# Performance work log

Measured on AMD Instinct MI355X. Metric: run time of the kernel, lower is better.

Reference implementation:

```python
import jax, jax.numpy as jnp
import numpy as np

H = 1024
A = H // 2
B = 32
S = 1024
T = 1024


def setup_inputs() -> dict:
    key = jax.random.key(0)
    ks = jax.random.split(key, 16)
    sc = 0.02
    inp = {
        "hidden": jax.random.normal(ks[0], (1, B, H), jnp.float32),
        "encoder_hiddens": jax.random.normal(ks[1], (S, B, H), jnp.float32),
        "h0_s": jax.random.normal(ks[2], (T, B, H), jnp.float32),
        "ax": jax.random.uniform(ks[3], (B, S, 1), jnp.float32),
        # weights: torch Linear(in,out,bias=False) -> W has shape [out,in], y = x @ W.T
        "W1": jax.random.normal(ks[4], (A, H), jnp.float32) * sc,
        "W2": jax.random.normal(ks[5], (A, H), jnp.float32) * sc,
        "W3": jax.random.normal(ks[6], (A, 1), jnp.float32) * sc,
        "W4": jax.random.normal(ks[7], (1, 3 * A), jnp.float32) * sc,
        "W5": jax.random.normal(ks[8], (A, H), jnp.float32) * sc,
        "W6": jax.random.normal(ks[9], (A, H), jnp.float32) * sc,
        "W7": jax.random.normal(ks[10], (A, H), jnp.float32) * sc,
        "W8": jax.random.normal(ks[11], (1, 3 * A), jnp.float32) * sc,
        "W9": jax.random.normal(ks[12], (H, H), jnp.float32) * sc,
        "W10": jax.random.normal(ks[13], (H, H), jnp.float32) * sc,
        "W11": jax.random.normal(ks[14], (1, 2 * H), jnp.float32) * sc,
    }
    return inp


def reference(hidden, encoder_hiddens, h0_s, ax,
              W1, W2, W3, W4, W5, W6, W7, W8, W9, W10, W11):
    h = hidden[0]  # [B,H], hidden.squeeze(0)

    # ---- encoder (x) attention with coverage, vectorized over S ----
    wx = jnp.einsum('sbh,ah->sba', encoder_hiddens, W1)          # [S,B,A]
    wxy = h @ W2.T                                               # [B,A]
    # Linear3 on ax[:, j] ([B,1]): outer product with W3 column
    wxr = ax[:, :, 0][:, :, None] * W3[:, 0][None, None, :]       # [B,S,A]
    wxr = jnp.transpose(wxr, (1, 0, 2))                           # [S,B,A]
    cat_x = jnp.tanh(jnp.concatenate(
        [wx, jnp.broadcast_to(wxy, (S,) + wxy.shape), wxr], axis=-1))  # [S,B,3A]
    exi = jnp.einsum('sbc,oc->bso', cat_x, W4)                    # [B,S,1]
    axi = jax.nn.softmax(exi, axis=1)                             # [B,S,1]
    cxi = jnp.einsum('bs,sbh->bh', axi[:, :, 0], encoder_hiddens)  # [B,H]
    ax_new = ax + axi

    # ---- decoder-history (t) attention, vectorized over T ----
    wt = jnp.einsum('tbh,ah->tba', h0_s, W5)                      # [T,B,A]
    wtx = cxi @ W6.T                                              # [B,A]
    wty = h @ W7.T                                                # [B,A]
    Tn = h0_s.shape[0]
    cat_t = jnp.tanh(jnp.concatenate(
        [wt,
         jnp.broadcast_to(wtx, (Tn,) + wtx.shape),
         jnp.broadcast_to(wty, (Tn,) + wty.shape)], axis=-1))     # [T,B,3A]
    eti = jnp.einsum('tbc,oc->bto', cat_t, W8)                    # [B,T,1]
    ati = jax.nn.softmax(eti, axis=1)
    cti = jnp.einsum('bt,tbh->bh', ati[:, :, 0], h0_s)            # [B,H]

    # ---- gated fusion ----
    gxi = jnp.tanh(cxi @ W9.T)
    gti = jnp.tanh(cti @ W10.T)
    zi = jax.nn.sigmoid(jnp.concatenate([cxi, cti], axis=1) @ W11.T)  # [B,1]
    ci = zi * gxi + (1.0 - zi) * gti                              # [B,H]
    return ci, ax_new
```

## Files before the change

kernel.cpp:

```cpp
#include <hip/hip_runtime.h>
#include <hip/hip_bf16.h>

#define HH 1024
#define AA 512
#define BB 32
#define SS 1024
#define TN 1024
#define M_ENC (SS*BB)
#define M_TOT ((SS+TN)*BB)
#define NCH 8

#define ABUF 8192

typedef __attribute__((ext_vector_type(8))) short short8;
typedef __attribute__((ext_vector_type(4))) float f4;

union bfu { __hip_bfloat16 h; unsigned short u; };
__device__ __forceinline__ unsigned int f2bu(float x) {
  bfu t; t.h = __float2bfloat16(x); return (unsigned int)t.u;
}
__device__ __forceinline__ unsigned short f2b(float x) {
  bfu t; t.h = __float2bfloat16(x); return t.u;
}
__device__ __forceinline__ float tanh_fast(float x) {
  float e = __expf(2.f * x);
  return 1.f - 2.f / (e + 1.f);
}

__global__ void prep_all(const float* __restrict__ W1, const float* __restrict__ W5,
                         const float* __restrict__ W3, const float* __restrict__ W4,
                         unsigned short* __restrict__ W1c, unsigned short* __restrict__ W5c,
                         float* __restrict__ C) {
  if (blockIdx.x < 512) {
    const float* __restrict__ W = (blockIdx.x < 256) ? W1 : W5;
    unsigned short* __restrict__ Wc = (blockIdx.x < 256) ? W1c : W5c;
    const int t = (blockIdx.x & 255) * 256 + threadIdx.x;
    const int lane = t & 63;
    const int rg = (t >> 6) & 31;
    const int kb = t >> 11;
    const int row = rg * 16 + (lane & 15);
    const int k = kb * 32 + ((lane >> 4) << 3);
    const float* src = W + (size_t)row * HH + k;
    f4 v0 = *(const f4*)(src);
    f4 v1 = *(const f4*)(src + 4);
    short8 o;
    o[0] = f2b(v0[0]); o[1] = f2b(v0[1]); o[2] = f2b(v0[2]); o[3] = f2b(v0[3]);
    o[4] = f2b(v1[0]); o[5] = f2b(v1[1]); o[6] = f2b(v1[2]); o[7] = f2b(v1[3]);
    *(short8*)(Wc + (size_t)t * 8) = o;
  } else {
    __shared__ float r1[256], r3[256], r5[256];
    const int tp = threadIdx.x;
    float s1 = 0.f, s3 = 0.f, s5 = 0.f;
    for (int a = tp; a < AA; a += 256) {
      const float w = W3[a], u = W4[2 * AA + a];
      const float w2 = w * w;
      s1 += u * w; s3 += u * w * w2; s5 += u * w * w2 * w2;
    }
    r1[tp] = s1; r3[tp] = s3; r5[tp] = s5;
    __syncthreads();
    for (int off = 128; off > 0; off >>= 1) {
      if (tp < off) { r1[tp] += r1[tp + off]; r3[tp] += r3[tp + off]; r5[tp] += r5[tp + off]; }
      __syncthreads();
    }
    if (tp == 0) { C[0] = r1[0]; C[1] = -r3[0] / 3.f; C[2] = r5[0] * (2.f / 15.f); }
  }
}

__global__ __launch_bounds__(512, 4)
void e1_gemm(const float* __restrict__ enc, const float* __restrict__ h0,
             const unsigned short* __restrict__ W1c, const unsigned short* __restrict__ W5c,
             const float* __restrict__ W4, const float* __restrict__ W8,
             float* __restrict__ e1s, float* __restrict__ e1t) {
  const int wg   = blockIdx.x;
  const int tid  = threadIdx.x;
  const int lane = tid & 63;
  const int colg = tid >> 6;
  const int l15  = lane & 15;
  const int lg   = lane >> 4;
  const int koff = (wg & 1) << 3;

  const bool is_enc = (wg * 64) < M_ENC;
  const float* __restrict__ Xg = is_enc ? enc : h0;
  const unsigned short* __restrict__ Wc = is_enc ? W1c : W5c;
  const float* __restrict__ Vg = is_enc ? W4 : W8;
  const int row0 = is_enc ? wg * 64 : wg * 64 - M_ENC;

  __shared__ char lds_raw[2 * ABUF];
  float* lred = (float*)lds_raw;

  f4 acc[4][4];
#pragma unroll
  for (int i = 0; i < 4; ++i)
#pragma unroll
    for (int j = 0; j < 4; ++j) acc[i][j] = (f4){0.f, 0.f, 0.f, 0.f};

  const int arow = tid >> 3;
  const int aq   = tid & 7;
  const float* ap = Xg + (size_t)(row0 + arow) * HH + aq * 4;
  const int slotS = (aq >> 1) ^ ((arow >> 1) & 3);
  const int aDst = arow * 64 + slotS * 16 + (aq & 1) * 8;

  const int aRd = l15 * 64 + ((lg ^ ((l15 >> 1) & 3)) << 4);

  const char* bp = (const char*)Wc + colg * 4096 + lane * 16;

  f4 an0, an1;
  short8 bfr[8];

#define ALOAD(k_) do {                                                        \
    an0 = *(const f4*)(ap + (k_) * 64);                                       \
    an1 = *(const f4*)(ap + (k_) * 64 + 32);                                  \
  } while (0)

#define AWR(bo_) do {                                                         \
    uint2 o0_, o1_;                                                           \
    o0_.x = f2bu(an0[0]) | (f2bu(an0[1]) << 16);                              \
    o0_.y = f2bu(an0[2]) | (f2bu(an0[3]) << 16);                              \
    o1_.x = f2bu(an1[0]) | (f2bu(an1[1]) << 16);                              \
    o1_.y = f2bu(an1[2]) | (f2bu(an1[3]) << 16);                              \
    *(uint2*)(lds_raw + (bo_) + aDst) = o0_;                                  \
    *(uint2*)(lds_raw + (bo_) + 4096 + aDst) = o1_;                           \
  } while (0)

#define BLOAD(kb2_) do {                                                      \
    const char* b_ = bp + (size_t)(kb2_) * 65536;                             \
    _Pragma("unroll")                                                         \
    for (int q_ = 0; q_ < 8; ++q_)                                            \
      bfr[q_] = *(const short8*)(b_ + (q_ >> 2) * 32768 + (q_ & 3) * 1024);   \
  } while (0)

#define COMPUTE(bo_) do {                                                     \
    const char* base_ = lds_raw + (bo_);                                      \
    _Pragma("unroll")                                                         \
    for (int ks_ = 0; ks_ < 2; ++ks_) {                                       \
      __builtin_amdgcn_s_setprio(1);                                          \
      _Pragma("unroll")                                                       \
      for (int rt = 0; rt < 4; ++rt) {                                        \
        short8 af_ = *(const short8*)(base_ + ks_ * 4096 + aRd + rt * 1024);  \
        _Pragma("unroll")                                                     \
        for (int cf = 0; cf < 4; ++cf)                                        \
          acc[rt][cf] = __builtin_amdgcn_mfma_f32_16x16x32_bf16(              \
              af_, bfr[ks_ * 4 + cf], acc[rt][cf], 0, 0, 0);                  \
      }                                                                       \
      __builtin_amdgcn_s_setprio(0);                                          \
    }                                                                         \
  } while (0)

#define SYNCA() do {                                                          \
    __builtin_amdgcn_sched_barrier(0);                                        \
    asm volatile("s_waitcnt lgkmcnt(0)" ::: "memory");                        \
    __builtin_amdgcn_s_barrier();                                             \
    __builtin_amdgcn_sched_barrier(0);                                        \
  } while (0)

  ALOAD(koff);
  AWR(0);
  ALOAD((1 + koff) & 15);
  SYNCA();

#pragma unroll 1
  for (int it = 0; it < 7; ++it) {
    const int kc0 = (2 * it + koff) & 15;
    const int ka2 = (2 * it + 2 + koff) & 15;
    const int kc1 = (2 * it + 1 + koff) & 15;
    const int ka3 = (2 * it + 3 + koff) & 15;
    AWR(ABUF); ALOAD(ka2); BLOAD(kc0); COMPUTE(0); SYNCA();
    AWR(0); ALOAD(ka3); BLOAD(kc1); COMPUTE(ABUF); SYNCA();
  }
  AWR(ABUF); BLOAD((14 + koff) & 15); COMPUTE(0); SYNCA();
  BLOAD((15 + koff) & 15); COMPUTE(ABUF);
#undef ALOAD
#undef AWR
#undef BLOAD
#undef COMPUTE
#undef SYNCA

  float vvv[4];
#pragma unroll
  for (int cf = 0; cf < 4; ++cf) vvv[cf] = Vg[colg * 64 + cf * 16 + l15];

  __syncthreads();
#pragma unroll
  for (int rt = 0; rt < 4; ++rt) {
    float ps[4] = {0.f, 0.f, 0.f, 0.f};
#pragma unroll
    for (int cf = 0; cf < 4; ++cf) {
      const float w = vvv[cf];
#pragma unroll
      for (int r = 0; r < 4; ++r) ps[r] += w * tanh_fast(acc[rt][cf][r]);
    }
#pragma unroll
    for (int r = 0; r < 4; ++r) {
#pragma unroll
      for (int off = 1; off < 16; off <<= 1) ps[r] += __shfl_xor(ps[r], off);
    }
    if (l15 == 0) {
#pragma unroll
      for (int r = 0; r < 4; ++r)
        lred[colg * 64 + rt * 16 + lg * 4 + r] = ps[r];
    }
  }
  __syncthreads();
  if (tid < 64) {
    float s = 0.f;
#pragma unroll
    for (int c = 0; c < 8; ++c) s += lred[c * 64 + tid];
    const int gr = row0 + tid;
    const int q = gr >> 5;
    const int b = gr & 31;
    if (is_enc) e1s[b * SS + q] = s;
    else        e1t[b * TN + q] = s;
  }
}

__global__ void softmax_both(const float* __restrict__ e1s, const float* __restrict__ e1t,
                             const float* __restrict__ ax, const float* __restrict__ C,
                             float* __restrict__ axi, float* __restrict__ ati,
                             float* __restrict__ axnew) {
  const int tid = threadIdx.x;
  __shared__ float red[256];
  if (blockIdx.x < BB) {
    const int b = blockIdx.x;
    const float c0 = C[0], c1 = C[1], c2 = C[2];
    float loc[4], xv[4];
    float m = -1e30f;
#pragma unroll
    for (int i = 0; i < 4; ++i) {
      const int s = i * 256 + tid;
      const float x = ax[b * SS + s];
      const float x2 = x * x;
      xv[i] = x;
      loc[i] = e1s[b * SS + s] + x * (c0 + x2 * (c1 + x2 * c2));
      m = fmaxf(m, loc[i]);
    }
    red[tid] = m; __syncthreads();
    for (int off = 128; off > 0; off >>= 1) {
      if (tid < off) red[tid] = fmaxf(red[tid], red[tid + off]);
      __syncthreads();
    }
    m = red[0]; __syncthreads();
    float sum = 0.f;
#pragma unroll
    for (int i = 0; i < 4; ++i) { loc[i] = __expf(loc[i] - m); sum += loc[i]; }
    red[tid] = sum; __syncthreads();
    for (int off = 128; off > 0; off >>= 1) {
      if (tid < off) red[tid] += red[tid + off];
      __syncthreads();
    }
    const float inv = 1.f / red[0];
#pragma unroll
    for (int i = 0; i < 4; ++i) {
      const int s = i * 256 + tid;
      const float a_ = loc[i] * inv;
      axi[b * SS + s] = a_;
      axnew[b * SS + s] = xv[i] + a_;
    }
  } else {
    const int b = blockIdx.x - BB;
    float loc[4];
    float m = -1e30f;
#pragma unroll
    for (int i = 0; i < 4; ++i) { loc[i] = e1t[b * TN + i * 256 + tid]; m = fmaxf(m, loc[i]); }
    red[tid] = m; __syncthreads();
    for (int off = 128; off > 0; off >>= 1) {
      if (tid < off) red[tid] = fmaxf(red[tid], red[tid + off]);
      __syncthreads();
    }
    m = red[0]; __syncthreads();
    float sum = 0.f;
#pragma unroll
    for (int i = 0; i < 4; ++i) { loc[i] = __expf(loc[i] - m); sum += loc[i]; }
    red[tid] = sum; __syncthreads();
    for (int off = 128; off > 0; off >>= 1) {
      if (tid < off) red[tid] += red[tid + off];
      __syncthreads();
    }
    const float inv = 1.f / red[0];
#pragma unroll
    for (int i = 0; i < 4; ++i) ati[b * TN + (i * 256 + tid)] = loc[i] * inv;
  }
}

__global__ void wpart2(const float* __restrict__ enc, const float* __restrict__ h0,
                       const float* __restrict__ axi, const float* __restrict__ ati,
                       float* __restrict__ partx, float* __restrict__ partt) {
  const int gb = blockIdx.x;
  const bool isx = gb < BB * NCH;
  const float* __restrict__ X = isx ? enc : h0;
  const float* __restrict__ w = isx ? axi : ati;
  float* __restrict__ part = isx ? partx : partt;
  const int idx = isx ? gb : gb - BB * NCH;
  const int b = idx / NCH, ch = idx % NCH;
  const int tid = threadIdx.x;
  __shared__ float ws[SS / NCH];
  if (tid < SS / NCH) ws[tid] = w[b * SS + ch * (SS / NCH) + tid];
  __syncthreads();
  f4 acc = (f4){0.f, 0.f, 0.f, 0.f};
  const float* base = X + ((size_t)(ch * (SS / NCH)) * BB + b) * HH + tid * 4;
#pragma unroll 4
  for (int i = 0; i < SS / NCH; ++i) {
    f4 x = *(const f4*)(base + (size_t)i * BB * HH);
    acc += ws[i] * x;
  }
  *(f4*)&part[((size_t)(b * NCH + ch)) * HH + tid * 4] = acc;
}

__global__ void wreduce2(const float* __restrict__ partx, const float* __restrict__ partt,
                         float* __restrict__ cxi, float* __restrict__ cti) {
  const int idx = blockIdx.x * 256 + threadIdx.x;
  const bool isx = idx < BB * HH;
  const float* __restrict__ part = isx ? partx : partt;
  float* __restrict__ outp = isx ? cxi : cti;
  const int j = isx ? idx : idx - BB * HH;
  const int b = j / HH, h = j % HH;
  float s = 0.f;
#pragma unroll
  for (int ch = 0; ch < NCH; ++ch) s += part[((size_t)(b * NCH + ch)) * HH + h];
  outp[j] = s;
}

__global__ void ci_kernel(const float* __restrict__ cxi, const float* __restrict__ cti,
                          const float* __restrict__ W9, const float* __restrict__ W10,
                          const float* __restrict__ W11, float* __restrict__ out_ci) {
  const int b = blockIdx.x >> 2, hb = blockIdx.x & 3, tid = threadIdx.x;
  const int h = hb * 256 + tid;
  __shared__ float cx[HH], ct[HH];
  __shared__ float zred[4];
  for (int i = tid; i < HH; i += 256) { cx[i] = cxi[b * HH + i]; ct[i] = cti[b * HH + i]; }
  __syncthreads();
  float zs = 0.f;
  for (int i = tid; i < HH; i += 256) zs += cx[i] * W11[i] + ct[i] * W11[HH + i];
  for (int off = 32; off > 0; off >>= 1) zs += __shfl_down(zs, off);
  if ((tid & 63) == 0) zred[tid >> 6] = zs;
  __syncthreads();
  const float zt = zred[0] + zred[1] + zred[2] + zred[3];
  const float z = 1.f / (1.f + __expf(-zt));

  const float* __restrict__ w9r  = W9  + (size_t)h * HH;
  const float* __restrict__ w10r = W10 + (size_t)h * HH;
  float gx = 0.f, gt = 0.f;
  for (int k = 0; k < HH; k += 4) {
    f4 a = *(const f4*)(w9r + k);
    f4 c = *(const f4*)(w10r + k);
    gx += cx[k] * a[0] + cx[k + 1] * a[1] + cx[k + 2] * a[2] + cx[k + 3] * a[3];
    gt += ct[k] * c[0] + ct[k + 1] * c[1] + ct[k + 2] * c[2] + ct[k + 3] * c[3];
  }
  out_ci[b * HH + h] = z * tanhf(gx) + (1.f - z) * tanhf(gt);
}

extern "C" void kernel_launch(void* const* d_in, const int* in_sizes, int n_in,
                              void* d_out, int out_size, void* d_ws, size_t ws_size,
                              hipStream_t stream) {
  const float* enc = (const float*)d_in[1];
  const float* h0  = (const float*)d_in[2];
  const float* ax  = (const float*)d_in[3];
  const float* W1  = (const float*)d_in[4];
  const float* W3  = (const float*)d_in[6];
  const float* W4  = (const float*)d_in[7];
  const float* W5  = (const float*)d_in[8];
  const float* W8  = (const float*)d_in[11];
  const float* W9  = (const float*)d_in[12];
  const float* W10 = (const float*)d_in[13];
  const float* W11 = (const float*)d_in[14];
  float* out = (float*)d_out;

  float* w = (float*)d_ws;
  unsigned short* W1c = (unsigned short*)w;
  unsigned short* W5c = (unsigned short*)(w + 262144);
  float* partx = w;
  float* partt = w + 262144;
  float* e1s   = w + 524288;
  float* e1t   = w + 557056;
  float* axi   = w + 589824;
  float* ati   = w + 622592;
  float* cxi   = w + 655360;
  float* cti   = w + 688128;
  float* Cpoly = w + 720896;

  prep_all<<<513, 256, 0, stream>>>(W1, W5, W3, W4, W1c, W5c, Cpoly);
  e1_gemm<<<M_TOT / 64, 512, 0, stream>>>(enc, h0, W1c, W5c, W4, W8, e1s, e1t);
  softmax_both<<<2 * BB, 256, 0, stream>>>(e1s, e1t, ax, Cpoly, axi, ati, out + BB * HH);
  wpart2<<<2 * BB * NCH, 256, 0, stream>>>(enc, h0, axi, ati, partx, partt);
  wreduce2<<<2 * BB * HH / 256, 256, 0, stream>>>(partx, partt, cxi, cti);
  ci_kernel<<<BB * 4, 256, 0, stream>>>(cxi, cti, W9, W10, W11, out);
}
```

Measured before the change: 209.5 us.

## Load A fragments directly from global into registers, dropping LDS staging

The GEMM in e1_gemm no longer stages the fp32 activation tile into a double-buffered LDS area with barriers. Each wave now reads its own A rows straight from global memory, converts them to bf16 in registers and feeds the MFMAs. The per-WG K-offset staggering is removed and launch bounds drop to 2 waves per SIMD to allow more registers. This removes LDS traffic and barriers, but all 8 waves in a workgroup now reload the same A rows from global/L2 (8x redundant reads), and occupancy is reduced.

```diff
diff --git a/kernel.cpp b/kernel.cpp
--- a/kernel.cpp
+++ b/kernel.cpp
@@ -9,8 +9,6 @@
 #define M_ENC (SS*BB)
 #define M_TOT ((SS+TN)*BB)
 #define NCH 8
-
-#define ABUF 8192
 
 typedef __attribute__((ext_vector_type(8))) short short8;
 typedef __attribute__((ext_vector_type(4))) float f4;
@@ -66,7 +64,7 @@
   }
 }
 
-__global__ __launch_bounds__(512, 4)
+__global__ __launch_bounds__(512, 2)
 void e1_gemm(const float* __restrict__ enc, const float* __restrict__ h0,
              const unsigned short* __restrict__ W1c, const unsigned short* __restrict__ W5c,
              const float* __restrict__ W4, const float* __restrict__ W8,
@@ -77,7 +75,6 @@
   const int colg = tid >> 6;
   const int l15  = lane & 15;
   const int lg   = lane >> 4;
-  const int koff = (wg & 1) << 3;
 
   const bool is_enc = (wg * 64) < M_ENC;
   const float* __restrict__ Xg = is_enc ? enc : h0;
@@ -85,8 +82,7 @@
   const float* __restrict__ Vg = is_enc ? W4 : W8;
   const int row0 = is_enc ? wg * 64 : wg * 64 - M_ENC;
 
-  __shared__ char lds_raw[2 * ABUF];
-  float* lred = (float*)lds_raw;
+  __shared__ float lred[512];
 
   f4 acc[4][4];
 #pragma unroll
@@ -94,92 +90,56 @@
 #pragma unroll
     for (int j = 0; j < 4; ++j) acc[i][j] = (f4){0.f, 0.f, 0.f, 0.f};
 
-  const int arow = tid >> 3;
-  const int aq   = tid & 7;
-  const float* ap = Xg + (size_t)(row0 + arow) * HH + aq * 4;
-  const int slotS = (aq >> 1) ^ ((arow >> 1) & 3);
-  const int aDst = arow * 64 + slotS * 16 + (aq & 1) * 8;
-
-  const int aRd = l15 * 64 + ((lg ^ ((l15 >> 1) & 3)) << 4);
+  const float* ap0 = Xg + (size_t)(row0 + l15) * HH + lg * 8;
+  const float* ap1 = ap0 + 16 * HH;
+  const float* ap2 = ap1 + 16 * HH;
+  const float* ap3 = ap2 + 16 * HH;
 
   const char* bp = (const char*)Wc + colg * 4096 + lane * 16;
 
-  f4 an0, an1;
-  short8 bfr[8];
-
-#define ALOAD(k_) do {                                                        \
-    an0 = *(const f4*)(ap + (k_) * 64);                                       \
-    an1 = *(const f4*)(ap + (k_) * 64 + 32);                                  \
+#define PACK8(d_, x0_, x1_) do {                                              \
+    unsigned int lo0_ = f2bu(x0_[0]) | (f2bu(x0_[1]) << 16);                  \
+    unsigned int hi0_ = f2bu(x0_[2]) | (f2bu(x0_[3]) << 16);                  \
+    unsigned int lo1_ = f2bu(x1_[0]) | (f2bu(x1_[1]) << 16);                  \
+    unsigned int hi1_ = f2bu(x1_[2]) | (f2bu(x1_[3]) << 16);                  \
+    d_[0] = (short)(lo0_ & 0xffff); d_[1] = (short)(lo0_ >> 16);              \
+    d_[2] = (short)(hi0_ & 0xffff); d_[3] = (short)(hi0_ >> 16);              \
+    d_[4] = (short)(lo1_ & 0xffff); d_[5] = (short)(lo1_ >> 16);              \
+    d_[6] = (short)(hi1_ & 0xffff); d_[7] = (short)(hi1_ >> 16);              \
   } while (0)
 
-#define AWR(bo_) do {                                                         \
-    uint2 o0_, o1_;                                                           \
-    o0_.x = f2bu(an0[0]) | (f2bu(an0[1]) << 16);                              \
-    o0_.y = f2bu(an0[2]) | (f2bu(an0[3]) << 16);                              \
-    o1_.x = f2bu(an1[0]) | (f2bu(an1[1]) << 16);                              \
-    o1_.y = f2bu(an1[2]) | (f2bu(an1[3]) << 16);                              \
-    *(uint2*)(lds_raw + (bo_) + aDst) = o0_;                                  \
-    *(uint2*)(lds_raw + (bo_) + 4096 + aDst) = o1_;                           \
-  } while (0)
-
-#define BLOAD(kb2_) do {                                                      \
-    const char* b_ = bp + (size_t)(kb2_) * 65536;                             \
-    _Pragma("unroll")                                                         \
-    for (int q_ = 0; q_ < 8; ++q_)                                            \
-      bfr[q_] = *(const short8*)(b_ + (q_ >> 2) * 32768 + (q_ & 3) * 1024);   \
-  } while (0)
-
-#define COMPUTE(bo_) do {                                                     \
-    const char* base_ = lds_raw + (bo_);                                      \
-    _Pragma("unroll")                                                         \
-    for (int ks_ = 0; ks_ < 2; ++ks_) {                                       \
-      __builtin_amdgcn_s_setprio(1);                                          \
-      _Pragma("unroll")                                                       \
-      for (int rt = 0; rt < 4; ++rt) {                                        \
-        short8 af_ = *(const short8*)(base_ + ks_ * 4096 + aRd + rt * 1024);  \
-        _Pragma("unroll")                                                     \
-        for (int cf = 0; cf < 4; ++cf)                                        \
-          acc[rt][cf] = __builtin_amdgcn_mfma_f32_16x16x32_bf16(              \
-              af_, bfr[ks_ * 4 + cf], acc[rt][cf], 0, 0, 0);                  \
-      }                                                                       \
-      __builtin_amdgcn_s_setprio(0);                                          \
-    }                                                                         \
-  } while (0)
-
-#define SYNCA() do {                                                          \
-    __builtin_amdgcn_sched_barrier(0);                                        \
-    asm volatile("s_waitcnt lgkmcnt(0)" ::: "memory");                        \
-    __builtin_amdgcn_s_barrier();                                             \
-    __builtin_amdgcn_sched_barrier(0);                                        \
-  } while (0)
-
-  ALOAD(koff);
-  AWR(0);
-  ALOAD((1 + koff) & 15);
-  SYNCA();
-
-#pragma unroll 1
-  for (int it = 0; it < 7; ++it) {
-    const int kc0 = (2 * it + koff) & 15;
-    const int ka2 = (2 * it + 2 + koff) & 15;
-    const int kc1 = (2 * it + 1 + koff) & 15;
-    const int ka3 = (2 * it + 3 + koff) & 15;
-    AWR(ABUF); ALOAD(ka2); BLOAD(kc0); COMPUTE(0); SYNCA();
-    AWR(0); ALOAD(ka3); BLOAD(kc1); COMPUTE(ABUF); SYNCA();
-  }
-  AWR(ABUF); BLOAD((14 + koff) & 15); COMPUTE(0); SYNCA();
-  BLOAD((15 + koff) & 15); COMPUTE(ABUF);
-#undef ALOAD
-#undef AWR
-#undef BLOAD
-#undef COMPUTE
-#undef SYNCA
+#pragma unroll 4
+  for (int kb = 0; kb < 16; ++kb) {
+    short8 bfr[8];
+#pragma unroll
+    for (int q = 0; q < 8; ++q)
+      bfr[q] = *(const short8*)(bp + (size_t)kb * 65536 +
+                                (q >> 2) * 32768 + (q & 3) * 1024);
+#pragma unroll
+    for (int ks = 0; ks < 2; ++ks) {
+      const int ko = kb * 64 + ks * 32;
+      f4 x00 = *(const f4*)(ap0 + ko), x01 = *(const f4*)(ap0 + ko + 4);
+      f4 x10 = *(const f4*)(ap1 + ko), x11 = *(const f4*)(ap1 + ko + 4);
+      f4 x20 = *(const f4*)(ap2 + ko), x21 = *(const f4*)(ap2 + ko + 4);
+      f4 x30 = *(const f4*)(ap3 + ko), x31 = *(const f4*)(ap3 + ko + 4);
+      short8 a0, a1, a2, a3;
+      PACK8(a0, x00, x01); PACK8(a1, x10, x11);
+      PACK8(a2, x20, x21); PACK8(a3, x30, x31);
+#pragma unroll
+      for (int cf = 0; cf < 4; ++cf) {
+        acc[0][cf] = __builtin_amdgcn_mfma_f32_16x16x32_bf16(a0, bfr[ks * 4 + cf], acc[0][cf], 0, 0, 0);
+        acc[1][cf] = __builtin_amdgcn_mfma_f32_16x16x32_bf16(a1, bfr[ks * 4 + cf], acc[1][cf], 0, 0, 0);
+        acc[2][cf] = __builtin_amdgcn_mfma_f32_16x16x32_bf16(a2, bfr[ks * 4 + cf], acc[2][cf], 0, 0, 0);
+        acc[3][cf] = __builtin_amdgcn_mfma_f32_16x16x32_bf16(a3, bfr[ks * 4 + cf], acc[3][cf], 0, 0, 0);
+      }
+    }
+  }
+#undef PACK8
 
   float vvv[4];
 #pragma unroll
   for (int cf = 0; cf < 4; ++cf) vvv[cf] = Vg[colg * 64 + cf * 16 + l15];
 
-  __syncthreads();
 #pragma unroll
   for (int rt = 0; rt < 4; ++rt) {
     float ps[4] = {0.f, 0.f, 0.f, 0.f};
```

Result: slower. 457.7 us (+118.5%).
